# Kernel tuning notes

Measured on AMD Instinct MI355X. Metric: run time of the kernel, lower is better.

The kernel has to match this reference:

```python
import jax, jax.numpy as jnp
import numpy as np

MIN_NORM = 1e-15
PROJ_EPS = 4e-3  # fp32 eps used by hgcn PoincareBall


def _artanh(x):
    x = jnp.clip(x, -1.0 + 1e-7, 1.0 - 1e-7)
    return 0.5 * jnp.log((1.0 + x) / (1.0 - x))


def _norm(x):
    return jnp.maximum(jnp.linalg.norm(x, axis=-1, keepdims=True), MIN_NORM)


def proj(x, c):
    norm = _norm(x)
    maxnorm = (1.0 - PROJ_EPS) / jnp.sqrt(c)
    return jnp.where(norm > maxnorm, x / norm * maxnorm, x)


def expmap0(u, c):
    sqrt_c = jnp.sqrt(c)
    u_norm = _norm(u)
    return jnp.tanh(sqrt_c * u_norm) * u / (sqrt_c * u_norm)


def logmap0(p, c):
    sqrt_c = jnp.sqrt(c)
    p_norm = _norm(p)
    return _artanh(sqrt_c * p_norm) * p / (sqrt_c * p_norm)


def mobius_add(x, y, c):
    x2 = jnp.sum(x * x, axis=-1, keepdims=True)
    y2 = jnp.sum(y * y, axis=-1, keepdims=True)
    xy = jnp.sum(x * y, axis=-1, keepdims=True)
    num = (1.0 + 2.0 * c * xy + c * y2) * x + (1.0 - c * x2) * y
    denom = 1.0 + 2.0 * c * xy + c * c * x2 * y2
    return num / jnp.maximum(denom, MIN_NORM)


def mobius_matvec(m, x, c):
    sqrt_c = jnp.sqrt(c)
    x_norm = _norm(x)
    mx = x @ m.T  # [N, out]
    mx_norm = _norm(mx)
    res_c = jnp.tanh(mx_norm / x_norm * _artanh(sqrt_c * x_norm)) * mx / (mx_norm * sqrt_c)
    cond = jnp.all(mx == 0.0, axis=-1, keepdims=True)
    return jnp.where(cond, jnp.zeros_like(res_c), res_c)


def setup_inputs() -> dict:
    key = jax.random.key(0)
    k1, k2, k3 = jax.random.split(key, 3)
    N, D = 8192, 256
    c = 1.0
    x = 0.05 * jax.random.normal(k1, (N, D), dtype=jnp.float32)
    x = proj(x, c)  # valid points on the Poincare ball
    # sparse-ish row-normalized adjacency, materialized densely
    a = (jax.random.uniform(k2, (N, N)) < 0.004).astype(jnp.float32)
    a = a + jnp.eye(N, dtype=jnp.float32)
    adj = a / jnp.sum(a, axis=-1, keepdims=True)
    gain = np.sqrt(2.0)
    bound = gain * np.sqrt(6.0 / (D + D))  # xavier_uniform with gain sqrt(2)
    weight = jax.random.uniform(k3, (D, D), minval=-bound, maxval=bound, dtype=jnp.float32)
    bias = jnp.zeros((D,), dtype=jnp.float32)
    return {"x": x, "adj": adj, "weight": weight, "bias": bias}


def reference(x, adj, weight, bias):
    c_in = jnp.float32(1.0)
    c_out = jnp.float32(1.0)
    # HypLinear (dropout=0, eval mode)
    mv = mobius_matvec(weight, x, c_in)
    res = proj(mv, c_in)
    hyp_bias = proj(expmap0(bias[None, :], c_in), c_in)  # proj_tan0 is identity
    h = proj(mobius_add(res, hyp_bias, c_in), c_in)
    # HypAgg (use_att=False): tangent-space neighborhood aggregation
    x_tangent = logmap0(h, c_in)
    support_t = adj @ x_tangent
    h = proj(expmap0(support_t, c_in), c_in)
    # HypAct
    xt = jax.nn.relu(logmap0(h, c_in))
    h = proj(expmap0(xt, c_out), c_out)
    return (h, adj)
```

## Files before the change

### kernel.cpp

```cpp
#include <hip/hip_runtime.h>
#include <hip/hip_bf16.h>

#define N_NODES 8192
#define D_DIM   256

typedef __attribute__((ext_vector_type(8))) short short8v;
typedef __attribute__((ext_vector_type(4))) float f32x4;

__device__ __forceinline__ float artanh_clip(float x) {
    x = fminf(x, 1.0f - 1e-7f);
    return 0.5f * logf((1.0f + x) / (1.0f - x));
}

__device__ __forceinline__ ushort4 cvt4_bf16(float4 v) {
    ushort4 b;
    b.x = __bfloat16_as_ushort(__float2bfloat16(v.x));
    b.y = __bfloat16_as_ushort(__float2bfloat16(v.y));
    b.z = __bfloat16_as_ushort(__float2bfloat16(v.z));
    b.w = __bfloat16_as_ushort(__float2bfloat16(v.w));
    return b;
}

__device__ __forceinline__ unsigned int pk2_bf16(float a, float b) {
    unsigned int lo = (unsigned int)__bfloat16_as_ushort(__float2bfloat16(a));
    unsigned int hi = (unsigned int)__bfloat16_as_ushort(__float2bfloat16(b));
    return lo | (hi << 16);
}

__device__ __forceinline__ void nt_store4(float4 v, float* p) {
    f32x4 w = {v.x, v.y, v.z, v.w};
    __builtin_nontemporal_store(w, (f32x4*)p);
}

__global__ void k0_bias(const float* __restrict__ bias, float* __restrict__ hbg) {
    __shared__ float sp[4];
    __shared__ float s_g;
    int t = threadIdx.x;
    float u = bias[t];
    float v = u * u;
    #pragma unroll
    for (int o = 1; o < 64; o <<= 1) v += __shfl_xor(v, o);
    if ((t & 63) == 0) sp[t >> 6] = v;
    __syncthreads();
    if (t == 0) {
        float s  = sp[0] + sp[1] + sp[2] + sp[3];
        float un = fmaxf(sqrtf(s), 1e-15f);
        float t1 = tanhf(un);
        s_g = (t1 > 0.996f) ? (0.996f / un) : (t1 / un);
    }
    __syncthreads();
    float hb = s_g * u;
    hbg[t] = hb;
    float v2 = hb * hb;
    #pragma unroll
    for (int o = 1; o < 64; o <<= 1) v2 += __shfl_xor(v2, o);
    if ((t & 63) == 0) sp[t >> 6] = v2;
    __syncthreads();
    if (t == 0) hbg[256] = sp[0] + sp[1] + sp[2] + sp[3];
}

__global__ __launch_bounds__(256) void k1_hyplinear(
    const float* __restrict__ x, const float* __restrict__ W,
    const float* __restrict__ hbg, __hip_bfloat16* __restrict__ xtT)
{
    __shared__ __align__(16) float sx[16][264];
    __shared__ __align__(16) float sw[256][36];
    __shared__ float s_xn[16], s_P[16], s_Q[16];
    __shared__ float s_hb[256];
    __shared__ float s_b2;

    const int t  = threadIdx.x;
    const int r0 = blockIdx.x * 16;
    const int row = t >> 4;
    const int j16 = (t & 15) * 4;

    {
        #pragma unroll
        for (int i = 0; i < 4; i++)
            *(float4*)(&sx[row][j16 + 64 * i]) =
                *(const float4*)(x + (r0 + row) * 256 + j16 + 64 * i);
    }
    s_hb[t] = hbg[t];
    if (t == 0) s_b2 = hbg[256];
    __syncthreads();

    {
        int r = t >> 4, j = t & 15;
        float s2 = 0.f;
        #pragma unroll
        for (int i = 0; i < 16; i++) { float v = sx[r][j + 16 * i]; s2 += v * v; }
        s2 += __shfl_xor(s2, 1); s2 += __shfl_xor(s2, 2);
        s2 += __shfl_xor(s2, 4); s2 += __shfl_xor(s2, 8);
        if (j == 0) s_xn[r] = s2;
    }

    float acc[16];
    #pragma unroll
    for (int r = 0; r < 16; r++) acc[r] = 0.f;

    for (int kc = 0; kc < 8; kc++) {
        __syncthreads();
        {
            int c4 = (t & 7) * 4;
            #pragma unroll
            for (int i = 0; i < 8; i++) {
                int d = i * 32 + (t >> 3);
                *(float4*)(&sw[d][c4]) = *(const float4*)(W + d * 256 + kc * 32 + c4);
            }
        }
        __syncthreads();
        #pragma unroll
        for (int kk = 0; kk < 8; kk++) {
            float4 w4 = *(const float4*)(&sw[t][kk * 4]);
            #pragma unroll
            for (int r = 0; r < 16; r++) {
                float4 x4 = *(const float4*)(&sx[r][kc * 32 + kk * 4]);
                acc[r] = fmaf(x4.x, w4.x, acc[r]);
                acc[r] = fmaf(x4.y, w4.y, acc[r]);
                acc[r] = fmaf(x4.z, w4.z, acc[r]);
                acc[r] = fmaf(x4.w, w4.w, acc[r]);
            }
        }
    }
    __syncthreads();
    #pragma unroll
    for (int r = 0; r < 16; r++) sx[r][t] = acc[r];
    __syncthreads();

    {
        int r = t >> 4, j = t & 15;
        float s2 = 0.f, dt = 0.f;
        #pragma unroll
        for (int i = 0; i < 16; i++) {
            float v = sx[r][j + 16 * i];
            s2 += v * v;
            dt += v * s_hb[j + 16 * i];
        }
        s2 += __shfl_xor(s2, 1); s2 += __shfl_xor(s2, 2);
        s2 += __shfl_xor(s2, 4); s2 += __shfl_xor(s2, 8);
        dt += __shfl_xor(dt, 1); dt += __shfl_xor(dt, 2);
        dt += __shfl_xor(dt, 4); dt += __shfl_xor(dt, 8);
        if (j == 0) {
            float b2  = s_b2;
            float xn  = fmaxf(sqrtf(s_xn[r]), 1e-15f);
            float mx2 = s2;
            float mxn = fmaxf(sqrtf(mx2), 1e-15f);
            float at = artanh_clip(xn);
            float tt = tanhf(mxn / xn * at);
            float fr = tt / mxn;
            if (tt > 0.996f) fr = 0.996f / mxn;
            float mvn = fminf(tt, 0.996f);
            float x2  = mvn * mvn;
            float xy  = fr * dt;
            float cA  = 1.0f + 2.0f * xy + b2;
            float cB  = 1.0f - x2;
            float den = fmaxf(1.0f + 2.0f * xy + x2 * b2, 1e-15f);
            float P0 = cA * fr / den;
            float Q0 = cB / den;
            float hn = sqrtf(fmaxf(P0 * P0 * mx2 + 2.0f * P0 * Q0 * dt + Q0 * Q0 * b2, 0.0f));
            hn = fmaxf(hn, 1e-15f);
            float pf  = (hn > 0.996f) ? (0.996f / hn) : 1.0f;
            float hnp = fminf(hn, 0.996f);
            float lam = artanh_clip(hnp) / hnp;
            s_P[r] = lam * pf * P0;
            s_Q[r] = lam * pf * Q0;
        }
    }
    __syncthreads();

    {
        float hb = s_hb[t];
        unsigned int pk[8];
        #pragma unroll
        for (int r = 0; r < 16; r += 2) {
            float a0 = s_P[r]     * acc[r]     + s_Q[r]     * hb;
            float a1 = s_P[r + 1] * acc[r + 1] + s_Q[r + 1] * hb;
            pk[r >> 1] = pk2_bf16(a0, a1);
        }
        uint4* dst = (uint4*)(xtT + t * 8192 + r0);
        dst[0] = make_uint4(pk[0], pk[1], pk[2], pk[3]);
        dst[1] = make_uint4(pk[4], pk[5], pk[6], pk[7]);
    }
}

__global__ __launch_bounds__(512, 6) void k2_gemm(
    const float* __restrict__ adj,
    const __hip_bfloat16* __restrict__ xtT,
    float* __restrict__ out_h,
    float* __restrict__ out_adj,
    float* __restrict__ part)
{
    __shared__ __align__(16) __hip_bfloat16 As[2][32][136];

    const int t     = threadIdx.x;
    const int lane  = t & 63;
    const int wave  = t >> 6;
    const int wr    = wave >> 2;
    const int wc    = wave & 3;
    const int bx    = blockIdx.x;
    const int m0    = (bx >> 2) * 32;
    const int s     = bx & 3;
    const int kbase = s * 2048;

    const int srow = t >> 4;
    const int sj   = t & 15;
    const float* aptr = adj     + (size_t)(m0 + srow) * 8192 + kbase + sj * 4;
    float*       optr = out_adj + (size_t)(m0 + srow) * 8192 + kbase + sj * 4;

    const int arow = lane & 15;
    const int g8   = 8 * (lane >> 4);
    const __hip_bfloat16* bbase =
        xtT + (size_t)(wc * 64 + arow) * 8192 + kbase + wr * 32 + g8;

    f32x4 acc[2][4];
    #pragma unroll
    for (int i = 0; i < 2; i++)
        #pragma unroll
        for (int j = 0; j < 4; j++) acc[i][j] = (f32x4){0.f, 0.f, 0.f, 0.f};

    float4 T0, T1;
    T0 = *(const float4*)(aptr);
    T1 = *(const float4*)(aptr + 64);
    nt_store4(T0, optr);
    nt_store4(T1, optr + 64);
    *(ushort4*)(&As[0][srow][sj * 4])      = cvt4_bf16(T0);
    *(ushort4*)(&As[0][srow][64 + sj * 4]) = cvt4_bf16(T1);
    __syncthreads();

    int cur = 0;
    for (int kt = 0; kt < 16; kt++) {
        const bool hn = (kt + 1 < 16);
        if (hn) {
            T0 = *(const float4*)(aptr + (kt + 1) * 128);
            T1 = *(const float4*)(aptr + (kt + 1) * 128 + 64);
        }

        #pragma unroll
        for (int sub = 0; sub < 2; sub++) {
            const int kcol = kt * 128 + sub * 64;
            short8v bf0 = *(const short8v*)(bbase + kcol);
            short8v bf1 = *(const short8v*)(bbase + (size_t)16 * 8192 + kcol);
            short8v bf2 = *(const short8v*)(bbase + (size_t)32 * 8192 + kcol);
            short8v bf3 = *(const short8v*)(bbase + (size_t)48 * 8192 + kcol);
            short8v a0  = *(const short8v*)(&As[cur][arow][sub * 64 + wr * 32 + g8]);
            short8v a1  = *(const short8v*)(&As[cur][16 + arow][sub * 64 + wr * 32 + g8]);

            acc[0][0] = __builtin_amdgcn_mfma_f32_16x16x32_bf16(a0, bf0, acc[0][0], 0, 0, 0);
            acc[0][1] = __builtin_amdgcn_mfma_f32_16x16x32_bf16(a0, bf1, acc[0][1], 0, 0, 0);
            acc[0][2] = __builtin_amdgcn_mfma_f32_16x16x32_bf16(a0, bf2, acc[0][2], 0, 0, 0);
            acc[0][3] = __builtin_amdgcn_mfma_f32_16x16x32_bf16(a0, bf3, acc[0][3], 0, 0, 0);
            acc[1][0] = __builtin_amdgcn_mfma_f32_16x16x32_bf16(a1, bf0, acc[1][0], 0, 0, 0);
            acc[1][1] = __builtin_amdgcn_mfma_f32_16x16x32_bf16(a1, bf1, acc[1][1], 0, 0, 0);
            acc[1][2] = __builtin_amdgcn_mfma_f32_16x16x32_bf16(a1, bf2, acc[1][2], 0, 0, 0);
            acc[1][3] = __builtin_amdgcn_mfma_f32_16x16x32_bf16(a1, bf3, acc[1][3], 0, 0, 0);
        }

        if (hn) {
            nt_store4(T0, optr + (kt + 1) * 128);
            nt_store4(T1, optr + (kt + 1) * 128 + 64);
            *(ushort4*)(&As[cur ^ 1][srow][sj * 4])      = cvt4_bf16(T0);
            *(ushort4*)(&As[cur ^ 1][srow][64 + sj * 4]) = cvt4_bf16(T1);
        }
        __syncthreads();
        cur ^= 1;
    }

    const int crow0 = 4 * (lane >> 4);
    const int ccol  = lane & 15;
    if (part) {
        float* pb = part + (size_t)(s * 2 + wr) * N_NODES * D_DIM;
        #pragma unroll
        for (int mf = 0; mf < 2; mf++)
            #pragma unroll
            for (int nf = 0; nf < 4; nf++)
                #pragma unroll
                for (int q = 0; q < 4; q++)
                    pb[(size_t)(m0 + mf * 16 + crow0 + q) * 256
                       + wc * 64 + nf * 16 + ccol] = acc[mf][nf][q];
    } else {
        #pragma unroll
        for (int mf = 0; mf < 2; mf++)
            #pragma unroll
            for (int nf = 0; nf < 4; nf++)
                #pragma unroll
                for (int q = 0; q < 4; q++)
                    atomicAdd(out_h + (size_t)(m0 + mf * 16 + crow0 + q) * 256
                              + wc * 64 + nf * 16 + ccol, acc[mf][nf][q]);
    }
}

__global__ __launch_bounds__(256) void k3_epilogue(
    float* __restrict__ h, const float* __restrict__ part)
{
    const int t = threadIdx.x;
    const int r = blockIdx.x * 16 + (t >> 4);
    const int j = t & 15;
    float* p = h + (size_t)r * 256 + j * 16;

    float4 v[4];
    if (part) {
        const size_t base = (size_t)r * 256 + j * 16;
        const size_t slab = (size_t)N_NODES * D_DIM;
        #pragma unroll
        for (int i = 0; i < 4; i++) {
            float4 a = *(const float4*)(part + base + 4 * i);
            #pragma unroll
            for (int sl = 1; sl < 8; sl++) {
                float4 b = *(const float4*)(part + sl * slab + base + 4 * i);
                a.x += b.x; a.y += b.y; a.z += b.z; a.w += b.w;
            }
            v[i] = a;
        }
    } else {
        #pragma unroll
        for (int i = 0; i < 4; i++) v[i] = *(const float4*)(p + 4 * i);
    }

    float s2 = 0.f, sp = 0.f;
    #pragma unroll
    for (int i = 0; i < 4; i++) {
        s2 += v[i].x * v[i].x + v[i].y * v[i].y + v[i].z * v[i].z + v[i].w * v[i].w;
        float px = fmaxf(v[i].x, 0.f), py = fmaxf(v[i].y, 0.f);
        float pz = fmaxf(v[i].z, 0.f), pw = fmaxf(v[i].w, 0.f);
        sp += px * px + py * py + pz * pz + pw * pw;
    }
    s2 += __shfl_xor(s2, 1); s2 += __shfl_xor(s2, 2); s2 += __shfl_xor(s2, 4); s2 += __shfl_xor(s2, 8);
    sp += __shfl_xor(sp, 1); sp += __shfl_xor(sp, 2); sp += __shfl_xor(sp, 4); sp += __shfl_xor(sp, 8);

    float ns = fmaxf(sqrtf(s2), 1e-15f);
    float t1 = tanhf(ns);
    float alpha = (t1 > 0.996f) ? (0.996f / ns) : (t1 / ns);
    float nh = fminf(t1, 0.996f);
    float beta = artanh_clip(nh) / nh;
    float ba = beta * alpha;
    float nxt = fmaxf(ba * sqrtf(sp), 1e-15f);
    float t2 = tanhf(nxt);
    float delta = (t2 > 0.996f) ? (0.996f / nxt) : (t2 / nxt);
    float F = delta * ba;

    #pragma unroll
    for (int i = 0; i < 4; i++) {
        float4 o;
        o.x = F * fmaxf(v[i].x, 0.f);
        o.y = F * fmaxf(v[i].y, 0.f);
        o.z = F * fmaxf(v[i].z, 0.f);
        o.w = F * fmaxf(v[i].w, 0.f);
        *(float4*)(p + 4 * i) = o;
    }
}

extern "C" void kernel_launch(void* const* d_in, const int* in_sizes, int n_in,
                              void* d_out, int out_size, void* d_ws, size_t ws_size,
                              hipStream_t stream)
{
    const float* x    = (const float*)d_in[0];
    const float* adj  = (const float*)d_in[1];
    const float* W    = (const float*)d_in[2];
    const float* bias = (const float*)d_in[3];

    float* out_h   = (float*)d_out;
    float* out_adj = out_h + (size_t)N_NODES * D_DIM;

    const size_t xtT_bytes = (size_t)D_DIM * N_NODES * 2;
    __hip_bfloat16* xtT = (__hip_bfloat16*)d_ws;
    float* hbg = (float*)((char*)d_ws + xtT_bytes);

    const size_t part_off   = xtT_bytes + 4096;
    const size_t part_bytes = (size_t)8 * N_NODES * D_DIM * sizeof(float);
    const bool use_part = ws_size >= part_off + part_bytes;
    float* part = use_part ? (float*)((char*)d_ws + part_off) : nullptr;

    k0_bias<<<1, 256, 0, stream>>>(bias, hbg);
    k1_hyplinear<<<512, 256, 0, stream>>>(x, W, hbg, xtT);
    if (!use_part)
        hipMemsetAsync(out_h, 0, (size_t)N_NODES * D_DIM * sizeof(float), stream);
    k2_gemm<<<1024, 512, 0, stream>>>(adj, xtT, out_h, out_adj, part);
    k3_epilogue<<<512, 256, 0, stream>>>(out_h, part);
}
```

Before: 307.3 us.

## Retile adjacency GEMM to 128-row tiles with 8-way K split

The adjacency×features GEMM now uses 128×256 output tiles per block with an 8-way split over K (1024 columns each) instead of 32-row tiles with a 4-way split. Each block runs half as many blocks, and each B fragment loaded from global memory is reused across four M fragments, cutting redundant reads of the bf16 feature matrix. The cost is twice the accumulator registers, lower occupancy (launch bound min-blocks hint removed), and still eight partial slabs for the epilogue to reduce.

```diff
diff --git a/kernel.cpp b/kernel.cpp
--- a/kernel.cpp
+++ b/kernel.cpp
@@ -183,83 +183,85 @@
     }
 }
 
-__global__ __launch_bounds__(512, 6) void k2_gemm(
+__global__ __launch_bounds__(512) void k2_gemm(
     const float* __restrict__ adj,
     const __hip_bfloat16* __restrict__ xtT,
     float* __restrict__ out_h,
     float* __restrict__ out_adj,
     float* __restrict__ part)
 {
-    __shared__ __align__(16) __hip_bfloat16 As[2][32][136];
+    __shared__ __align__(16) __hip_bfloat16 As[2][128][72];
 
     const int t     = threadIdx.x;
     const int lane  = t & 63;
     const int wave  = t >> 6;
-    const int wr    = wave >> 2;
-    const int wc    = wave & 3;
+    const int wm    = wave >> 2;
+    const int wn    = wave & 3;
     const int bx    = blockIdx.x;
-    const int m0    = (bx >> 2) * 32;
-    const int s     = bx & 3;
-    const int kbase = s * 2048;
-
-    const int srow = t >> 4;
-    const int sj   = t & 15;
-    const float* aptr = adj     + (size_t)(m0 + srow) * 8192 + kbase + sj * 4;
-    float*       optr = out_adj + (size_t)(m0 + srow) * 8192 + kbase + sj * 4;
+    const int m0    = (bx >> 3) * 128;
+    const int s     = bx & 7;
+    const int kbase = s * 1024;
+
+    const int srow = t >> 2;
+    const int sc   = (t & 3) * 16;
+    const float* aptr = adj     + (size_t)(m0 + srow) * 8192 + kbase + sc;
+    float*       optr = out_adj + (size_t)(m0 + srow) * 8192 + kbase + sc;
 
     const int arow = lane & 15;
-    const int g8   = 8 * (lane >> 4);
+    const int g8   = lane >> 4;
     const __hip_bfloat16* bbase =
-        xtT + (size_t)(wc * 64 + arow) * 8192 + kbase + wr * 32 + g8;
-
-    f32x4 acc[2][4];
-    #pragma unroll
-    for (int i = 0; i < 2; i++)
+        xtT + (size_t)(wn * 64 + arow) * 8192 + kbase + g8 * 8;
+
+    f32x4 acc[4][4];
+    #pragma unroll
+    for (int i = 0; i < 4; i++)
         #pragma unroll
         for (int j = 0; j < 4; j++) acc[i][j] = (f32x4){0.f, 0.f, 0.f, 0.f};
 
-    float4 T0, T1;
-    T0 = *(const float4*)(aptr);
-    T1 = *(const float4*)(aptr + 64);
-    nt_store4(T0, optr);
-    nt_store4(T1, optr + 64);
-    *(ushort4*)(&As[0][srow][sj * 4])      = cvt4_bf16(T0);
-    *(ushort4*)(&As[0][srow][64 + sj * 4]) = cvt4_bf16(T1);
+    float4 T[4];
+    #pragma unroll
+    for (int i = 0; i < 4; i++) T[i] = *(const float4*)(aptr + i * 4);
+    #pragma unroll
+    for (int i = 0; i < 4; i++) nt_store4(T[i], optr + i * 4);
+    #pragma unroll
+    for (int i = 0; i < 4; i++)
+        *(ushort4*)(&As[0][srow][sc + i * 4]) = cvt4_bf16(T[i]);
     __syncthreads();
 
     int cur = 0;
     for (int kt = 0; kt < 16; kt++) {
         const bool hn = (kt + 1 < 16);
         if (hn) {
-            T0 = *(const float4*)(aptr + (kt + 1) * 128);
-            T1 = *(const float4*)(aptr + (kt + 1) * 128 + 64);
+            #pragma unroll
+            for (int i = 0; i < 4; i++)
+                T[i] = *(const float4*)(aptr + (kt + 1) * 64 + i * 4);
         }
 
         #pragma unroll
         for (int sub = 0; sub < 2; sub++) {
-            const int kcol = kt * 128 + sub * 64;
-            short8v bf0 = *(const short8v*)(bbase + kcol);
-            short8v bf1 = *(const short8v*)(bbase + (size_t)16 * 8192 + kcol);
-            short8v bf2 = *(const short8v*)(bbase + (size_t)32 * 8192 + kcol);
-            short8v bf3 = *(const short8v*)(bbase + (size_t)48 * 8192 + kcol);
-            short8v a0  = *(const short8v*)(&As[cur][arow][sub * 64 + wr * 32 + g8]);
-            short8v a1  = *(const short8v*)(&As[cur][16 + arow][sub * 64 + wr * 32 + g8]);
-
-            acc[0][0] = __builtin_amdgcn_mfma_f32_16x16x32_bf16(a0, bf0, acc[0][0], 0, 0, 0);
-            acc[0][1] = __builtin_amdgcn_mfma_f32_16x16x32_bf16(a0, bf1, acc[0][1], 0, 0, 0);
-            acc[0][2] = __builtin_amdgcn_mfma_f32_16x16x32_bf16(a0, bf2, acc[0][2], 0, 0, 0);
-            acc[0][3] = __builtin_amdgcn_mfma_f32_16x16x32_bf16(a0, bf3, acc[0][3], 0, 0, 0);
-            acc[1][0] = __builtin_amdgcn_mfma_f32_16x16x32_bf16(a1, bf0, acc[1][0], 0, 0, 0);
-            acc[1][1] = __builtin_amdgcn_mfma_f32_16x16x32_bf16(a1, bf1, acc[1][1], 0, 0, 0);
-            acc[1][2] = __builtin_amdgcn_mfma_f32_16x16x32_bf16(a1, bf2, acc[1][2], 0, 0, 0);
-            acc[1][3] = __builtin_amdgcn_mfma_f32_16x16x32_bf16(a1, bf3, acc[1][3], 0, 0, 0);
+            const int kcol = kt * 64 + sub * 32;
+            short8v bf[4];
+            #pragma unroll
+            for (int nf = 0; nf < 4; nf++)
+                bf[nf] = *(const short8v*)(bbase + (size_t)(nf * 16) * 8192 + kcol);
+            #pragma unroll
+            for (int mf = 0; mf < 4; mf++) {
+                short8v af = *(const short8v*)(
+                    &As[cur][wm * 64 + mf * 16 + arow][sub * 32 + g8 * 8]);
+                #pragma unroll
+                for (int nf = 0; nf < 4; nf++)
+                    acc[mf][nf] = __builtin_amdgcn_mfma_f32_16x16x32_bf16(
+                        af, bf[nf], acc[mf][nf], 0, 0, 0);
+            }
         }
 
         if (hn) {
-            nt_store4(T0, optr + (kt + 1) * 128);
-            nt_store4(T1, optr + (kt + 1) * 128 + 64);
-            *(ushort4*)(&As[cur ^ 1][srow][sj * 4])      = cvt4_bf16(T0);
-            *(ushort4*)(&As[cur ^ 1][srow][64 + sj * 4]) = cvt4_bf16(T1);
+            #pragma unroll
+            for (int i = 0; i < 4; i++)
+                nt_store4(T[i], optr + (kt + 1) * 64 + i * 4);
+            #pragma unroll
+            for (int i = 0; i < 4; i++)
+                *(ushort4*)(&As[cur ^ 1][srow][sc + i * 4]) = cvt4_bf16(T[i]);
         }
         __syncthreads();
         cur ^= 1;
@@ -268,24 +270,24 @@
     const int crow0 = 4 * (lane >> 4);
     const int ccol  = lane & 15;
     if (part) {
-        float* pb = part + (size_t)(s * 2 + wr) * N_NODES * D_DIM;
-        #pragma unroll
-        for (int mf = 0; mf < 2; mf++)
+        float* pb = part + (size_t)s * N_NODES * D_DIM;
+        #pragma unroll
+        for (int mf = 0; mf < 4; mf++)
             #pragma unroll
             for (int nf = 0; nf < 4; nf++)
                 #pragma unroll
                 for (int q = 0; q < 4; q++)
-                    pb[(size_t)(m0 + mf * 16 + crow0 + q) * 256
-                       + wc * 64 + nf * 16 + ccol] = acc[mf][nf][q];
+                    pb[(size_t)(m0 + wm * 64 + mf * 16 + crow0 + q) * 256
+                       + wn * 64 + nf * 16 + ccol] = acc[mf][nf][q];
     } else {
         #pragma unroll
-        for (int mf = 0; mf < 2; mf++)
+        for (int mf = 0; mf < 4; mf++)
             #pragma unroll
             for (int nf = 0; nf < 4; nf++)
                 #pragma unroll
                 for (int q = 0; q < 4; q++)
-                    atomicAdd(out_h + (size_t)(m0 + mf * 16 + crow0 + q) * 256
-                              + wc * 64 + nf * 16 + ccol, acc[mf][nf][q]);
+                    atomicAdd(out_h + (size_t)(m0 + wm * 64 + mf * 16 + crow0 + q) * 256
+                              + wn * 64 + nf * 16 + ccol, acc[mf][nf][q]);
     }
 }
 
@@ -374,6 +376,6 @@
     k1_hyplinear<<<512, 256, 0, stream>>>(x, W, hbg, xtT);
     if (!use_part)
         hipMemsetAsync(out_h, 0, (size_t)N_NODES * D_DIM * sizeof(float), stream);
-    k2_gemm<<<1024, 512, 0, stream>>>(adj, xtT, out_h, out_adj, part);
+    k2_gemm<<<512, 512, 0, stream>>>(adj, xtT, out_h, out_adj, part);
     k3_epilogue<<<512, 256, 0, stream>>>(out_h, part);
 }
```

Result: slower. 667.7 us (+117.3%).
